# Optimization experiments

Hardware: AMD Instinct MI355X
Metric: run time of the kernel (lower is better)

Reference implementation:

```python
import jax, jax.numpy as jnp
import numpy as np
from jax import lax

B, L, K, OUT = 16384, 8192, 2, 128
L3 = L - 3 * (K - 1)  # 8189, length after 3 valid convs


def setup_inputs() -> dict:
    key = jax.random.key(0)
    ks = jax.random.split(key, 9)
    return {
        "x": jax.random.normal(ks[0], (B, 1, L), jnp.float32),
        "w1": jax.random.normal(ks[1], (1, 1, K), jnp.float32),
        "b1": jax.random.normal(ks[2], (1,), jnp.float32),
        "w2": jax.random.normal(ks[3], (1, 1, K), jnp.float32),
        "b2": jax.random.normal(ks[4], (1,), jnp.float32),
        "w3": jax.random.normal(ks[5], (1, 1, K), jnp.float32),
        "b3": jax.random.normal(ks[6], (1,), jnp.float32),
        "W": jax.random.normal(ks[7], (OUT, L3), jnp.float32) * 0.02,
        "b": jax.random.normal(ks[8], (OUT,), jnp.float32),
    }


def _conv1d(x, w, b):
    # x: [B, 1, L_in], w: [1, 1, K] (OIW), valid padding, stride 1
    y = lax.conv_general_dilated(x, w, window_strides=(1,), padding="VALID",
                                 dimension_numbers=("NCW", "OIW", "NCW"))
    return y + b[None, :, None]


def reference(x, w1, b1, w2, b2, w3, b3, W, b):
    h = jax.nn.relu(_conv1d(x, w1, b1))
    h = jax.nn.relu(_conv1d(h, w2, b2))
    h = jax.nn.relu(_conv1d(h, w3, b3))
    flat = h.reshape(h.shape[0], -1)          # [B, L3]
    return flat @ W.T + b                     # [B, OUT]
```

## Files before the change

### kernel.cpp

```cpp
#include <hip/hip_runtime.h>
#include <hip/hip_bf16.h>

typedef __attribute__((ext_vector_type(8))) short short8;
typedef __attribute__((ext_vector_type(8))) unsigned short ushort8;
typedef __attribute__((ext_vector_type(4))) float f32x4;

#define LIN  8192
#define L3V  8189
#define NOUT 128
#define KP   8192
#define BM   64
#define BK   64
#define NT   (KP / BK)
#define PITCH (BK + 8)

static __device__ __forceinline__ unsigned short f2bf(float f) {
    union { float f; unsigned u; } c; c.f = f;
    unsigned r = c.u + 0x7FFFu + ((c.u >> 16) & 1u);
    return (unsigned short)(r >> 16);
}

__global__ void wprep(const float* __restrict__ W, unsigned short* __restrict__ Wb) {
    int idx = blockIdx.x * 256 + threadIdx.x;
    int n = idx >> 13;
    int k = idx & (KP - 1);
    float v = (k < L3V) ? W[(size_t)n * L3V + k] : 0.0f;
    Wb[idx] = f2bf(v);
}

__global__ __launch_bounds__(512, 4) void fused(
    const float* __restrict__ x,
    const float* __restrict__ w1, const float* __restrict__ b1,
    const float* __restrict__ w2, const float* __restrict__ b2,
    const float* __restrict__ w3, const float* __restrict__ b3,
    const unsigned short* __restrict__ Wb,
    const float* __restrict__ bias,
    float* __restrict__ out)
{
    __shared__ unsigned short hA[2][BM * PITCH];
    __shared__ unsigned short wA[2][NOUT * PITCH];

    const int tid  = threadIdx.x;
    const int row0 = blockIdx.x * BM;

    const float w10 = w1[0], w11 = w1[1], cb1 = b1[0];
    const float w20 = w2[0], w21 = w2[1], cb2 = b2[0];
    const float w30 = w3[0], w31 = w3[1], cb3 = b3[0];

    const int srow = tid >> 3;
    const int scol = (tid & 7) * 8;
    const float* xrow = x + (size_t)(row0 + srow) * LIN;

    const int wn = tid >> 2;
    const int wq = tid & 3;
    const unsigned short* wrow = Wb + (size_t)wn * KP + wq * 16;

    const int lane = tid & 63;
    const int wid  = tid >> 6;
    const int wr   = wid >> 1;
    const int wc   = wid & 1;
    const int l15  = lane & 15;
    const int koff = (lane >> 4) * 8;
    const int arow_off = (wr * 16 + l15) * PITCH + koff;

    f32x4 acc[4];
    #pragma unroll
    for (int f = 0; f < 4; ++f) acc[f] = (f32x4){0.f, 0.f, 0.f, 0.f};

    float   xv[12];
    ushort8 wv[2];

    auto stage_load = [&](int t) {
        const int gk = t * BK + scol;
        if (gk + 12 <= LIN) {
            #pragma unroll
            for (int q = 0; q < 3; ++q) {
                const float4 v = *reinterpret_cast<const float4*>(xrow + gk + q * 4);
                xv[q*4+0] = v.x; xv[q*4+1] = v.y; xv[q*4+2] = v.z; xv[q*4+3] = v.w;
            }
        } else {
            #pragma unroll
            for (int q = 0; q < 2; ++q) {
                const float4 v = *reinterpret_cast<const float4*>(xrow + gk + q * 4);
                xv[q*4+0] = v.x; xv[q*4+1] = v.y; xv[q*4+2] = v.z; xv[q*4+3] = v.w;
            }
            xv[8] = 0.f; xv[9] = 0.f; xv[10] = 0.f; xv[11] = 0.f;
        }
        const ushort8* wsrc = reinterpret_cast<const ushort8*>(wrow + t * BK);
        wv[0] = wsrc[0];
        wv[1] = wsrc[1];
    };

    auto stage_store = [&](int t, int s) {
        const int gk = t * BK + scol;
        float h1[10];
        #pragma unroll
        for (int j = 0; j < 10; ++j)
            h1[j] = fmaxf(fmaf(w10, xv[j], fmaf(w11, xv[j+1], cb1)), 0.0f);
        float h2[9];
        #pragma unroll
        for (int j = 0; j < 9; ++j)
            h2[j] = fmaxf(fmaf(w20, h1[j], fmaf(w21, h1[j+1], cb2)), 0.0f);
        ushort8 hp;
        #pragma unroll
        for (int j = 0; j < 8; ++j) {
            float h3 = fmaxf(fmaf(w30, h2[j], fmaf(w31, h2[j+1], cb3)), 0.0f);
            hp[j] = (gk + j < L3V) ? f2bf(h3) : (unsigned short)0;
        }
        *reinterpret_cast<ushort8*>(&hA[s][srow * PITCH + scol]) = hp;
        ushort8* wdst = reinterpret_cast<ushort8*>(&wA[s][wn * PITCH + wq * 16]);
        wdst[0] = wv[0];
        wdst[1] = wv[1];
    };

    auto mfma_tile = [&](int s) {
        const unsigned short* hB = hA[s];
        const unsigned short* wB = wA[s];
        #pragma unroll
        for (int kk = 0; kk < BK; kk += 32) {
            const short8 af = *reinterpret_cast<const short8*>(&hB[arow_off + kk]);
            #pragma unroll
            for (int f = 0; f < 4; ++f) {
                const int bn = wc * 64 + f * 16 + l15;
                const short8 bf = *reinterpret_cast<const short8*>(&wB[bn * PITCH + kk + koff]);
                acc[f] = __builtin_amdgcn_mfma_f32_16x16x32_bf16(af, bf, acc[f], 0, 0, 0);
            }
        }
    };

    stage_load(0);
    stage_store(0, 0);
    stage_load(1);
    __syncthreads();

    int sel = 0;
    #pragma unroll 1
    for (int t = 0; t < NT; ++t) {
        mfma_tile(sel);
        if (t + 1 < NT) stage_store(t + 1, sel ^ 1);
        if (t + 2 < NT) stage_load(t + 2);
        __syncthreads();
        sel ^= 1;
    }

    #pragma unroll
    for (int f = 0; f < 4; ++f) {
        const int col = wc * 64 + f * 16 + l15;
        const float bv = bias[col];
        #pragma unroll
        for (int j = 0; j < 4; ++j) {
            const int grow = row0 + wr * 16 + (lane >> 4) * 4 + j;
            out[(size_t)grow * NOUT + col] = acc[f][j] + bv;
        }
    }
}

extern "C" void kernel_launch(void* const* d_in, const int* in_sizes, int n_in,
                              void* d_out, int out_size, void* d_ws, size_t ws_size,
                              hipStream_t stream) {
    const float* x  = (const float*)d_in[0];
    const float* w1 = (const float*)d_in[1];
    const float* b1 = (const float*)d_in[2];
    const float* w2 = (const float*)d_in[3];
    const float* b2 = (const float*)d_in[4];
    const float* w3 = (const float*)d_in[5];
    const float* b3 = (const float*)d_in[6];
    const float* W  = (const float*)d_in[7];
    const float* b  = (const float*)d_in[8];
    float* out = (float*)d_out;
    unsigned short* Wb = (unsigned short*)d_ws;

    wprep<<<dim3((NOUT * KP) / 256), dim3(256), 0, stream>>>(W, Wb);
    fused<<<dim3(16384 / BM), dim3(512), 0, stream>>>(
        x, w1, b1, w2, b2, w3, b3, Wb, b, out);
}
```

Baseline: 154.7 us.

## Pre-swizzle W into MFMA fragment order and load B operands directly from global

The weight prep kernel now writes W in bf16, laid out in the exact per-lane fragment order used by the 16x16x32 MFMA. The main kernel loads B fragments straight from global/L2 instead of staging them through shared memory. The tile shape changes to 32 rows by 128 K, with 8 waves split as 2 rows by 4 column groups, and the weight LDS buffer is removed. This cuts LDS traffic and footprint and doubles the number of blocks. In exchange, every block re-reads the full W from L2 with no LDS reuse across waves, and the direct global loads may add latency on the MFMA path.

```diff
diff --git a/kernel.cpp b/kernel.cpp
--- a/kernel.cpp
+++ b/kernel.cpp
@@ -9,8 +9,8 @@
 #define L3V  8189
 #define NOUT 128
 #define KP   8192
-#define BM   64
-#define BK   64
+#define BM   32
+#define BK   128
 #define NT   (KP / BK)
 #define PITCH (BK + 8)
 
@@ -22,10 +22,19 @@
 
 __global__ void wprep(const float* __restrict__ W, unsigned short* __restrict__ Wb) {
     int idx = blockIdx.x * 256 + threadIdx.x;
-    int n = idx >> 13;
-    int k = idx & (KP - 1);
-    float v = (k < L3V) ? W[(size_t)n * L3V + k] : 0.0f;
-    Wb[idx] = f2bf(v);
+    const int lane = idx & 63;
+    const int s    = (idx >> 6) & 3;
+    const int g    = (idx >> 8) & 7;
+    const int t    = idx >> 11;
+    const int row  = g * 16 + (lane & 15);
+    const int k0   = t * BK + s * 32 + (lane >> 4) * 8;
+    ushort8 v;
+    #pragma unroll
+    for (int j = 0; j < 8; ++j) {
+        const int k = k0 + j;
+        v[j] = (k < L3V) ? f2bf(W[(size_t)row * L3V + k]) : (unsigned short)0;
+    }
+    *reinterpret_cast<ushort8*>(Wb + (size_t)idx * 8) = v;
 }
 
 __global__ __launch_bounds__(512, 4) void fused(
@@ -38,7 +47,6 @@
     float* __restrict__ out)
 {
     __shared__ unsigned short hA[2][BM * PITCH];
-    __shared__ unsigned short wA[2][NOUT * PITCH];
 
     const int tid  = threadIdx.x;
     const int row0 = blockIdx.x * BM;
@@ -47,28 +55,25 @@
     const float w20 = w2[0], w21 = w2[1], cb2 = b2[0];
     const float w30 = w3[0], w31 = w3[1], cb3 = b3[0];
 
-    const int srow = tid >> 3;
-    const int scol = (tid & 7) * 8;
+    const int srow = tid >> 4;
+    const int scol = (tid & 15) * 8;
     const float* xrow = x + (size_t)(row0 + srow) * LIN;
-
-    const int wn = tid >> 2;
-    const int wq = tid & 3;
-    const unsigned short* wrow = Wb + (size_t)wn * KP + wq * 16;
 
     const int lane = tid & 63;
     const int wid  = tid >> 6;
-    const int wr   = wid >> 1;
-    const int wc   = wid & 1;
+    const int wr   = wid >> 2;
+    const int wc   = wid & 3;
     const int l15  = lane & 15;
     const int koff = (lane >> 4) * 8;
     const int arow_off = (wr * 16 + l15) * PITCH + koff;
 
-    f32x4 acc[4];
-    #pragma unroll
-    for (int f = 0; f < 4; ++f) acc[f] = (f32x4){0.f, 0.f, 0.f, 0.f};
+    const unsigned short* wbase = Wb + ((size_t)(wc * 2) * 2048 + (size_t)lane * 8);
 
-    float   xv[12];
-    ushort8 wv[2];
+    f32x4 acc[2];
+    acc[0] = (f32x4){0.f, 0.f, 0.f, 0.f};
+    acc[1] = (f32x4){0.f, 0.f, 0.f, 0.f};
+
+    float xv[12];
 
     auto stage_load = [&](int t) {
         const int gk = t * BK + scol;
@@ -86,9 +91,6 @@
             }
             xv[8] = 0.f; xv[9] = 0.f; xv[10] = 0.f; xv[11] = 0.f;
         }
-        const ushort8* wsrc = reinterpret_cast<const ushort8*>(wrow + t * BK);
-        wv[0] = wsrc[0];
-        wv[1] = wsrc[1];
     };
 
     auto stage_store = [&](int t, int s) {
@@ -108,21 +110,17 @@
             hp[j] = (gk + j < L3V) ? f2bf(h3) : (unsigned short)0;
         }
         *reinterpret_cast<ushort8*>(&hA[s][srow * PITCH + scol]) = hp;
-        ushort8* wdst = reinterpret_cast<ushort8*>(&wA[s][wn * PITCH + wq * 16]);
-        wdst[0] = wv[0];
-        wdst[1] = wv[1];
     };
 
-    auto mfma_tile = [&](int s) {
+    auto mfma_tile = [&](int s, int t) {
         const unsigned short* hB = hA[s];
-        const unsigned short* wB = wA[s];
+        const unsigned short* wt = wbase + (size_t)t * 16384;
         #pragma unroll
-        for (int kk = 0; kk < BK; kk += 32) {
-            const short8 af = *reinterpret_cast<const short8*>(&hB[arow_off + kk]);
+        for (int ks = 0; ks < 4; ++ks) {
+            const short8 af = *reinterpret_cast<const short8*>(&hB[arow_off + ks * 32]);
             #pragma unroll
-            for (int f = 0; f < 4; ++f) {
-                const int bn = wc * 64 + f * 16 + l15;
-                const short8 bf = *reinterpret_cast<const short8*>(&wB[bn * PITCH + kk + koff]);
+            for (int f = 0; f < 2; ++f) {
+                const short8 bf = *reinterpret_cast<const short8*>(wt + f * 2048 + ks * 512);
                 acc[f] = __builtin_amdgcn_mfma_f32_16x16x32_bf16(af, bf, acc[f], 0, 0, 0);
             }
         }
@@ -136,7 +134,7 @@
     int sel = 0;
     #pragma unroll 1
     for (int t = 0; t < NT; ++t) {
-        mfma_tile(sel);
+        mfma_tile(sel, t);
         if (t + 1 < NT) stage_store(t + 1, sel ^ 1);
         if (t + 2 < NT) stage_load(t + 2);
         __syncthreads();
@@ -144,8 +142,8 @@
     }
 
     #pragma unroll
-    for (int f = 0; f < 4; ++f) {
-        const int col = wc * 64 + f * 16 + l15;
+    for (int f = 0; f < 2; ++f) {
+        const int col = wc * 32 + f * 16 + l15;
         const float bv = bias[col];
         #pragma unroll
         for (int j = 0; j < 4; ++j) {
@@ -170,7 +168,7 @@
     float* out = (float*)d_out;
     unsigned short* Wb = (unsigned short*)d_ws;
 
-    wprep<<<dim3((NOUT * KP) / 256), dim3(256), 0, stream>>>(W, Wb);
+    wprep<<<dim3(512), dim3(256), 0, stream>>>(W, Wb);
     fused<<<dim3(16384 / BM), dim3(512), 0, stream>>>(
         x, w1, b1, w2, b2, w3, b3, Wb, b, out);
 }
```

New measurement: 185.3 us. +19.7%, slower.

## Split K dimension across two blocks with partial-sum reduction kernel

Applied to the files above, without the earlier changes.

Launches the fused conv+GEMM kernel with a second grid dimension that splits the K range in half. Each half writes partial sums to a workspace, and a new reduce kernel adds the two halves plus bias. This doubles the block count from 256 to 512 to improve occupancy across CUs, at the cost of an extra 16 MB of partial-sum traffic and an extra kernel launch.

```diff
diff --git a/kernel.cpp b/kernel.cpp
--- a/kernel.cpp
+++ b/kernel.cpp
@@ -11,8 +11,9 @@
 #define KP   8192
 #define BM   64
 #define BK   64
-#define NT   (KP / BK)
+#define NTH  64
 #define PITCH (BK + 8)
+#define NROW 16384
 
 static __device__ __forceinline__ unsigned short f2bf(float f) {
     union { float f; unsigned u; } c; c.f = f;
@@ -28,20 +29,36 @@
     Wb[idx] = f2bf(v);
 }
 
+__global__ void reduce_out(const float* __restrict__ p,
+                           const float* __restrict__ bias,
+                           float* __restrict__ out) {
+    const int idx = blockIdx.x * 256 + threadIdx.x;
+    const float4 a = reinterpret_cast<const float4*>(p)[idx];
+    const float4 c = reinterpret_cast<const float4*>(p)[idx + (NROW * NOUT / 4)];
+    const float4 bb = *reinterpret_cast<const float4*>(bias + ((idx * 4) & (NOUT - 1)));
+    float4 o;
+    o.x = a.x + c.x + bb.x;
+    o.y = a.y + c.y + bb.y;
+    o.z = a.z + c.z + bb.z;
+    o.w = a.w + c.w + bb.w;
+    reinterpret_cast<float4*>(out)[idx] = o;
+}
+
 __global__ __launch_bounds__(512, 4) void fused(
     const float* __restrict__ x,
     const float* __restrict__ w1, const float* __restrict__ b1,
     const float* __restrict__ w2, const float* __restrict__ b2,
     const float* __restrict__ w3, const float* __restrict__ b3,
     const unsigned short* __restrict__ Wb,
-    const float* __restrict__ bias,
-    float* __restrict__ out)
+    float* __restrict__ part)
 {
     __shared__ unsigned short hA[2][BM * PITCH];
     __shared__ unsigned short wA[2][NOUT * PITCH];
 
     const int tid  = threadIdx.x;
     const int row0 = blockIdx.x * BM;
+    const int kh   = blockIdx.y;
+    const int tb   = kh * NTH;
 
     const float w10 = w1[0], w11 = w1[1], cb1 = b1[0];
     const float w20 = w2[0], w21 = w2[1], cb2 = b2[0];
@@ -71,7 +88,7 @@
     ushort8 wv[2];
 
     auto stage_load = [&](int t) {
-        const int gk = t * BK + scol;
+        const int gk = (tb + t) * BK + scol;
         if (gk + 12 <= LIN) {
             #pragma unroll
             for (int q = 0; q < 3; ++q) {
@@ -86,13 +103,13 @@
             }
             xv[8] = 0.f; xv[9] = 0.f; xv[10] = 0.f; xv[11] = 0.f;
         }
-        const ushort8* wsrc = reinterpret_cast<const ushort8*>(wrow + t * BK);
+        const ushort8* wsrc = reinterpret_cast<const ushort8*>(wrow + (tb + t) * BK);
         wv[0] = wsrc[0];
         wv[1] = wsrc[1];
     };
 
     auto stage_store = [&](int t, int s) {
-        const int gk = t * BK + scol;
+        const int gk = (tb + t) * BK + scol;
         float h1[10];
         #pragma unroll
         for (int j = 0; j < 10; ++j)
@@ -135,22 +152,22 @@
 
     int sel = 0;
     #pragma unroll 1
-    for (int t = 0; t < NT; ++t) {
+    for (int t = 0; t < NTH; ++t) {
         mfma_tile(sel);
-        if (t + 1 < NT) stage_store(t + 1, sel ^ 1);
-        if (t + 2 < NT) stage_load(t + 2);
+        if (t + 1 < NTH) stage_store(t + 1, sel ^ 1);
+        if (t + 2 < NTH) stage_load(t + 2);
         __syncthreads();
         sel ^= 1;
     }
 
+    float* pbase = part + (size_t)kh * NROW * NOUT;
     #pragma unroll
     for (int f = 0; f < 4; ++f) {
         const int col = wc * 64 + f * 16 + l15;
-        const float bv = bias[col];
         #pragma unroll
         for (int j = 0; j < 4; ++j) {
             const int grow = row0 + wr * 16 + (lane >> 4) * 4 + j;
-            out[(size_t)grow * NOUT + col] = acc[f][j] + bv;
+            pbase[(size_t)grow * NOUT + col] = acc[f][j];
         }
     }
 }
@@ -168,9 +185,12 @@
     const float* W  = (const float*)d_in[7];
     const float* b  = (const float*)d_in[8];
     float* out = (float*)d_out;
-    unsigned short* Wb = (unsigned short*)d_ws;
+
+    unsigned short* Wb   = (unsigned short*)d_ws;
+    float*          part = (float*)((char*)d_ws + (2u << 20));
 
     wprep<<<dim3((NOUT * KP) / 256), dim3(256), 0, stream>>>(W, Wb);
-    fused<<<dim3(16384 / BM), dim3(512), 0, stream>>>(
-        x, w1, b1, w2, b2, w3, b3, Wb, b, out);
+    fused<<<dim3(NROW / BM, 2), dim3(512), 0, stream>>>(
+        x, w1, b1, w2, b2, w3, b3, Wb, part);
+    reduce_out<<<dim3(NROW * NOUT / 4 / 256), dim3(256), 0, stream>>>(part, b, out);
 }
```

Result: faster. 146.0 us (-5.6%).
